# Performance work log

Measured on AMD Instinct MI355X. Metric: run time of the kernel, lower is better.

The kernel has to match this reference:

```python
import jax, jax.numpy as jnp
import numpy as np

N_USERS = 40000
N_POIS = 20000
D = 128
N_EDGES = 500000
N_LAYERS = 2
B = 256
NPOS = 100
TOPK = 20


def setup_inputs() -> dict:
    key = jax.random.key(0)
    ks = jax.random.split(key, 24)
    # guarantee every user row / poi col has at least one edge (avoids 0-norm rows)
    er = jnp.concatenate([jnp.arange(N_USERS, dtype=jnp.int32),
                          jax.random.randint(ks[0], (N_EDGES - N_USERS,), 0, N_USERS, jnp.int32)])
    ec = jnp.concatenate([jnp.arange(N_USERS, dtype=jnp.int32) % N_POIS,
                          jax.random.randint(ks[1], (N_EDGES - N_USERS,), 0, N_POIS, jnp.int32)])
    w0 = lambda k, shape: jax.random.normal(k, shape, jnp.float32) * 0.05
    return {
        'edge_row': er,
        'edge_col': ec,
        'click_vals': jax.random.uniform(ks[2], (N_EDGES,), jnp.float32),
        'favor_vals': jax.random.uniform(ks[3], (N_EDGES,), jnp.float32),
        'consume_vals': jax.random.uniform(ks[4], (N_EDGES,), jnp.float32),
        'uid_embed': w0(ks[5], (N_USERS, D)),
        'pid_embed': w0(ks[6], (N_POIS, D)),
        'user_index': jax.random.randint(ks[7], (B, 1), 0, N_USERS, jnp.int32),
        'poi_index': jax.random.randint(ks[8], (B, NPOS), 0, N_POIS, jnp.int32),
        'labels': (jax.random.uniform(ks[9], (B, NPOS)) < 0.5).astype(jnp.float32),
        'global_user_feature': w0(ks[10], (N_USERS, D)),
        'w': w0(ks[11], (1, 3)),
        'fw': w0(ks[12], (3, 1)),
        'W_user_click': w0(ks[13], (D, D)),
        'W_poi_click': w0(ks[14], (D, D)),
        'W_user_favor': w0(ks[15], (D, D)),
        'W_poi_favor': w0(ks[16], (D, D)),
        'W_user_consume': w0(ks[17], (D, D)),
        'W_poi_consume': w0(ks[18], (D, D)),
        'Ws': w0(ks[19], (D, D)),
        'bs_bias': w0(ks[20], (D,)),
    }


def reference(edge_row, edge_col, click_vals, favor_vals, consume_vals, uid_embed, pid_embed,
              user_index, poi_index, labels, global_user_feature, w, fw,
              W_user_click, W_poi_click, W_user_favor, W_poi_favor,
              W_user_consume, W_poi_consume, Ws, bs_bias):
    n_users, n_pois = uid_embed.shape[0], pid_embed.shape[0]
    batch_user = user_index.reshape(-1)

    def gcn(vals, Wu, Wp):
        # bipartite GCN propagation: A @ p (user side), A.T @ u (poi side)
        su, sp = uid_embed, pid_embed          # running sums of per-layer normalized features
        u, p = uid_embed, pid_embed            # un-normalized propagated features
        for _ in range(N_LAYERS):
            u = jax.ops.segment_sum(vals[:, None] * p[edge_col], edge_row, num_segments=n_users)
            su = su + u / jnp.linalg.norm(u, axis=1, keepdims=True)
            p = jax.ops.segment_sum(vals[:, None] * u[edge_row], edge_col, num_segments=n_pois)
            sp = sp + p / jnp.linalg.norm(p, axis=1, keepdims=True)
        uf = su @ Wu.T                         # final_user_linear (bias=False)
        pf = sp @ Wp.T                         # final_poi_linear (bias=False)
        return uf[batch_user] @ pf.T, uf       # [B, n_pois], [n_users, D]

    wn = jax.nn.softmax(w, axis=1)
    fwn = jax.nn.softmax(fw, axis=0)

    click_up, click_uf = gcn(click_vals, W_user_click, W_poi_click)
    favor_up, favor_uf = gcn(favor_vals + 1e-18 * click_vals, W_user_favor, W_poi_favor)
    consume_up, consume_uf = gcn(consume_vals + 1e-18 * click_vals, W_user_consume, W_poi_consume)

    alt = favor_up * wn[0, 0] + click_up * wn[0, 1] + consume_up * wn[0, 2]
    predict = jnp.take_along_axis(alt, poi_index, axis=1)                      # [B, NPOS]
    # BCEWithLogitsLoss (mean reduction), numerically stable form
    select_loss = jnp.mean(jax.nn.relu(predict) - predict * labels + jnp.log1p(jnp.exp(-jnp.abs(predict))))

    L = user_index.shape[1]
    cur = batch_user[jnp.arange(0, user_index.shape[0] * L, L)]                # first user of each row
    # gcn_user_feature stacked (favor, consume, click) @ fw
    id_feat = favor_uf * fwn[0, 0] + consume_uf * fwn[1, 0] + click_uf * fwn[2, 0]

    # Select_Layer (all inputs to matmuls are detached in the original)
    id_d = jax.lax.stop_gradient(id_feat)
    bs = id_d[cur] @ Ws.T + bs_bias
    uu = bs @ id_d.T                                                           # [B, n_users]
    top_score, top_idx = jax.lax.top_k(uu, TOPK)
    top_score = jax.nn.softmax(jax.lax.stop_gradient(top_score), axis=-1)
    neigh = jax.lax.stop_gradient(global_user_feature[top_idx])                # [B, TOPK, D]
    user_feature = jnp.einsum('bk,bkd->bd', top_score, neigh)
    return select_loss, user_feature
```

## Files before the change

kernel.cpp:

```cpp
#include <hip/hip_runtime.h>

#define N_USERS 40000
#define N_POIS  20000
#define DIM     128
#define N_EDGES 500000
#define BATCH   256
#define NPOS    100
#define TOPK    20
#define NCHUNK  128
#define CPT     313
#define SCHUNK  1024
#define RCH     40
#define CCH     20
#define LOSS_BLOCKS 25

typedef _Float16 f16x8 __attribute__((ext_vector_type(8)));
typedef float f32x4 __attribute__((ext_vector_type(4)));

__device__ __forceinline__ int iclamp(int x, int lo, int hi) {
    return x < lo ? lo : (x > hi ? hi : x);
}
__device__ __forceinline__ float2 h2f2(unsigned int u) {
    union { unsigned int u32; _Float16 h[2]; } v; v.u32 = u;
    return make_float2((float)v.h[0], (float)v.h[1]);
}
__device__ __forceinline__ unsigned int f2h2(float x, float y) {
    union { unsigned int u32; _Float16 h[2]; } v;
    v.h[0] = (_Float16)x; v.h[1] = (_Float16)y; return v.u32;
}
__device__ __forceinline__ float softmax3(const float* p, int sel) {
    float a0 = p[0], a1 = p[1], a2 = p[2];
    float m = fmaxf(a0, fmaxf(a1, a2));
    float e0 = expf(a0 - m), e1 = expf(a1 - m), e2 = expf(a2 - m);
    float den = e0 + e1 + e2;
    float e = (sel == 0) ? e0 : ((sel == 1) ? e1 : e2);
    return e / den;
}
template<int CH>
__device__ __forceinline__ float pickvT(int4 q) {
    return __int_as_float(CH == 0 ? q.y : (CH == 1 ? q.z : q.w));
}
__device__ __forceinline__ f16x8 frag8(const float* p) {
    float4 x = *(const float4*)(p);
    float4 y = *(const float4*)(p + 4);
    f16x8 f;
    f[0] = (_Float16)x.x; f[1] = (_Float16)x.y; f[2] = (_Float16)x.z; f[3] = (_Float16)x.w;
    f[4] = (_Float16)y.x; f[5] = (_Float16)y.y; f[6] = (_Float16)y.z; f[7] = (_Float16)y.w;
    return f;
}

__global__ void zero_kernel(unsigned int* __restrict__ p, int nwords) {
    int i = blockIdx.x * blockDim.x + threadIdx.x;
    if (i < nwords) p[i] = 0u;
}

__global__ void cast_f16_kernel(const float* __restrict__ src, unsigned short* __restrict__ dst,
                                int n2) {
    int i = blockIdx.x * blockDim.x + threadIdx.x;
    if (i < n2) {
        float2 v = *(const float2*)(src + 2 * (size_t)i);
        *(unsigned int*)(dst + 2 * (size_t)i) = f2h2(v.x, v.y);
    }
}

__global__ void hist_kernel(const int* __restrict__ er, const int* __restrict__ ec,
                            int* __restrict__ rcnt, int* __restrict__ ccnt,
                            int* __restrict__ rord, int* __restrict__ cord) {
    int e0 = 4 * (blockIdx.x * blockDim.x + threadIdx.x);
    if (e0 + 4 <= N_EDGES) {
        int4 r4 = *(const int4*)(er + e0);
        int4 c4 = *(const int4*)(ec + e0);
        int rr[4] = { r4.x, r4.y, r4.z, r4.w };
        int cc[4] = { c4.x, c4.y, c4.z, c4.w };
        int ro[4], co[4];
        #pragma unroll
        for (int j = 0; j < 4; j++) {
            ro[j] = atomicAdd(&rcnt[iclamp(rr[j], 0, N_USERS - 1)], 1);
            co[j] = atomicAdd(&ccnt[iclamp(cc[j], 0, N_POIS - 1)], 1);
        }
        *(int4*)(rord + e0) = make_int4(ro[0], ro[1], ro[2], ro[3]);
        *(int4*)(cord + e0) = make_int4(co[0], co[1], co[2], co[3]);
    } else {
        for (int e = e0; e < N_EDGES; e++) {
            rord[e] = atomicAdd(&rcnt[iclamp(er[e], 0, N_USERS - 1)], 1);
            cord[e] = atomicAdd(&ccnt[iclamp(ec[e], 0, N_POIS - 1)], 1);
        }
    }
}

__global__ void chunksum_kernel(const int* __restrict__ rcnt, const int* __restrict__ ccnt,
                                int* __restrict__ rsum, int* __restrict__ csum) {
    int side = blockIdx.y;
    const int* cnt = side ? ccnt : rcnt;
    int n = side ? N_POIS : N_USERS;
    int nch = side ? CCH : RCH;
    int b = blockIdx.x;
    if (b >= nch) return;
    int t = threadIdx.x;
    int i = b * SCHUNK + t * 4;
    int s = 0;
    if (i + 4 <= n) {
        int4 v = *(const int4*)(cnt + i);
        s = v.x + v.y + v.z + v.w;
    } else {
        for (int j = i; j < n; j++) s += cnt[j];
    }
    __shared__ int red[256];
    red[t] = s;
    __syncthreads();
    for (int o = 128; o > 0; o >>= 1) {
        if (t < o) red[t] += red[t + o];
        __syncthreads();
    }
    if (t == 0) (side ? csum : rsum)[b] = red[0];
}

__global__ void chunkscan_kernel(const int* __restrict__ rsum, const int* __restrict__ csum,
                                 int* __restrict__ rbase, int* __restrict__ cbase,
                                 int* __restrict__ rptr, int* __restrict__ cptr) {
    int w = threadIdx.x >> 6, l = threadIdx.x & 63;
    const int* src = w ? csum : rsum;
    int* dst = w ? cbase : rbase;
    int nch = w ? CCH : RCH;
    int orig = (l < nch) ? src[l] : 0;
    int v = orig;
    #pragma unroll
    for (int o = 1; o < 64; o <<= 1) {
        int u = __shfl_up(v, o, 64);
        if (l >= o) v += u;
    }
    if (l < nch) dst[l] = v - orig;
    if (l == nch - 1) {
        if (w) cptr[N_POIS] = v; else rptr[N_USERS] = v;
    }
}

__global__ void scatterscan_kernel(const int* __restrict__ rcnt, const int* __restrict__ ccnt,
                                   const int* __restrict__ rbase, const int* __restrict__ cbase,
                                   int* __restrict__ rptr, int* __restrict__ cptr) {
    int side = blockIdx.y;
    const int* cnt = side ? ccnt : rcnt;
    const int* basea = side ? cbase : rbase;
    int* ptr = side ? cptr : rptr;
    int n = side ? N_POIS : N_USERS;
    int nch = side ? CCH : RCH;
    int b = blockIdx.x;
    if (b >= nch) return;
    int t = threadIdx.x;
    int i = b * SCHUNK + t * 4;
    int c0 = 0, c1 = 0, c2 = 0, c3 = 0;
    if (i + 4 <= n) {
        int4 v = *(const int4*)(cnt + i);
        c0 = v.x; c1 = v.y; c2 = v.z; c3 = v.w;
    } else {
        if (i + 0 < n) c0 = cnt[i + 0];
        if (i + 1 < n) c1 = cnt[i + 1];
        if (i + 2 < n) c2 = cnt[i + 2];
    }
    int tsum = c0 + c1 + c2 + c3;
    int l = t & 63, w = t >> 6;
    int v = tsum;
    #pragma unroll
    for (int o = 1; o < 64; o <<= 1) {
        int u = __shfl_up(v, o, 64);
        if (l >= o) v += u;
    }
    __shared__ int wsum[4];
    if (l == 63) wsum[w] = v;
    __syncthreads();
    int wbase = 0;
    for (int k = 0; k < w; k++) wbase += wsum[k];
    int ex = v - tsum + wbase + basea[b];
    if (i + 4 <= n) {
        *(int4*)(ptr + i) = make_int4(ex, ex + c0, ex + c0 + c1, ex + c0 + c1 + c2);
    } else {
        if (i + 0 < n) ptr[i + 0] = ex;
        if (i + 1 < n) ptr[i + 1] = ex + c0;
        if (i + 2 < n) ptr[i + 2] = ex + c0 + c1;
    }
}

__global__ void fill_kernel(const int* __restrict__ er, const int* __restrict__ ec,
                            const int* __restrict__ rptr, const int* __restrict__ cptr,
                            const int* __restrict__ rord, const int* __restrict__ cord,
                            int4* __restrict__ rpack, int4* __restrict__ cpack,
                            const float* __restrict__ ck, const float* __restrict__ fv,
                            const float* __restrict__ cs) {
    int e0 = 4 * (blockIdx.x * blockDim.x + threadIdx.x);
    if (e0 + 4 <= N_EDGES) {
        int4 r4 = *(const int4*)(er + e0);
        int4 c4 = *(const int4*)(ec + e0);
        int4 ro4 = *(const int4*)(rord + e0);
        int4 co4 = *(const int4*)(cord + e0);
        float4 k4 = *(const float4*)(ck + e0);
        float4 f4 = *(const float4*)(fv + e0);
        float4 s4 = *(const float4*)(cs + e0);
        int rr[4] = { r4.x, r4.y, r4.z, r4.w };
        int cc[4] = { c4.x, c4.y, c4.z, c4.w };
        int ro[4] = { ro4.x, ro4.y, ro4.z, ro4.w };
        int co[4] = { co4.x, co4.y, co4.z, co4.w };
        float kk[4] = { k4.x, k4.y, k4.z, k4.w };
        float ff[4] = { f4.x, f4.y, f4.z, f4.w };
        float ss[4] = { s4.x, s4.y, s4.z, s4.w };
        #pragma unroll
        for (int j = 0; j < 4; j++) {
            int r = iclamp(rr[j], 0, N_USERS - 1), c = iclamp(cc[j], 0, N_POIS - 1);
            int v0 = __float_as_int(kk[j]);
            int v1 = __float_as_int(ff[j]);
            int v2 = __float_as_int(ss[j]);
            int pr = iclamp(rptr[r] + ro[j], 0, N_EDGES - 1);
            rpack[pr] = make_int4(c, v0, v1, v2);
            int pc = iclamp(cptr[c] + co[j], 0, N_EDGES - 1);
            cpack[pc] = make_int4(r, v0, v1, v2);
        }
    } else {
        for (int e = e0; e < N_EDGES; e++) {
            int r = iclamp(er[e], 0, N_USERS - 1), c = iclamp(ec[e], 0, N_POIS - 1);
            int v0 = __float_as_int(ck[e]);
            int v1 = __float_as_int(fv[e]);
            int v2 = __float_as_int(cs[e]);
            int pr = iclamp(rptr[r] + rord[e], 0, N_EDGES - 1);
            rpack[pr] = make_int4(c, v0, v1, v2);
            int pc = iclamp(cptr[c] + cord[e], 0, N_EDGES - 1);
            cpack[pc] = make_int4(r, v0, v1, v2);
        }
    }
}

template<int CH>
__global__ __launch_bounds__(256) void spmm_kernel(
        const int* __restrict__ ptr, const int4* __restrict__ pack,
        const unsigned short* __restrict__ src,
        unsigned short* __restrict__ raw_h,
        const float* __restrict__ base,
        float* __restrict__ acc, int nrows) {
    int wid = (blockIdx.x * blockDim.x + threadIdx.x) >> 6;
    int lane = threadIdx.x & 63;
    if (wid >= nrows) return;
    int beg = __builtin_amdgcn_readfirstlane(iclamp(ptr[wid], 0, N_EDGES));
    int end = __builtin_amdgcn_readfirstlane(iclamp(ptr[wid + 1], 0, N_EDGES));
    if (end < beg) end = beg;
    float ax = 0.f, ay = 0.f;
    int e = beg;
    int lo2 = lane * 2;
    for (; e + 8 <= end; e += 8) {
        int4 q0 = pack[e + 0], q1 = pack[e + 1], q2 = pack[e + 2], q3 = pack[e + 3];
        int4 q4 = pack[e + 4], q5 = pack[e + 5], q6 = pack[e + 6], q7 = pack[e + 7];
        float v0 = pickvT<CH>(q0), v1 = pickvT<CH>(q1), v2 = pickvT<CH>(q2), v3 = pickvT<CH>(q3);
        float v4 = pickvT<CH>(q4), v5 = pickvT<CH>(q5), v6 = pickvT<CH>(q6), v7 = pickvT<CH>(q7);
        float2 p0 = h2f2(*(const unsigned int*)(src + (size_t)q0.x * DIM + lo2));
        float2 p1 = h2f2(*(const unsigned int*)(src + (size_t)q1.x * DIM + lo2));
        float2 p2 = h2f2(*(const unsigned int*)(src + (size_t)q2.x * DIM + lo2));
        float2 p3 = h2f2(*(const unsigned int*)(src + (size_t)q3.x * DIM + lo2));
        float2 p4 = h2f2(*(const unsigned int*)(src + (size_t)q4.x * DIM + lo2));
        float2 p5 = h2f2(*(const unsigned int*)(src + (size_t)q5.x * DIM + lo2));
        float2 p6 = h2f2(*(const unsigned int*)(src + (size_t)q6.x * DIM + lo2));
        float2 p7 = h2f2(*(const unsigned int*)(src + (size_t)q7.x * DIM + lo2));
        ax = fmaf(v0, p0.x, fmaf(v1, p1.x, fmaf(v2, p2.x, fmaf(v3, p3.x, ax))));
        ax = fmaf(v4, p4.x, fmaf(v5, p5.x, fmaf(v6, p6.x, fmaf(v7, p7.x, ax))));
        ay = fmaf(v0, p0.y, fmaf(v1, p1.y, fmaf(v2, p2.y, fmaf(v3, p3.y, ay))));
        ay = fmaf(v4, p4.y, fmaf(v5, p5.y, fmaf(v6, p6.y, fmaf(v7, p7.y, ay))));
    }
    if (e < end) {
        int last = end - 1;
        int e1 = e + 1 <= last ? e + 1 : last;
        int e2 = e + 2 <= last ? e + 2 : last;
        int e3 = e + 3 <= last ? e + 3 : last;
        int e4 = e + 4 <= last ? e + 4 : last;
        int e5 = e + 5 <= last ? e + 5 : last;
        int e6 = e + 6 <= last ? e + 6 : last;
        int e7 = e + 7 <= last ? e + 7 : last;
        int4 q0 = pack[e], q1 = pack[e1], q2 = pack[e2], q3 = pack[e3];
        int4 q4 = pack[e4], q5 = pack[e5], q6 = pack[e6], q7 = pack[e7];
        float v0 = pickvT<CH>(q0);
        float v1 = (e + 1 < end) ? pickvT<CH>(q1) : 0.f;
        float v2 = (e + 2 < end) ? pickvT<CH>(q2) : 0.f;
        float v3 = (e + 3 < end) ? pickvT<CH>(q3) : 0.f;
        float v4 = (e + 4 < end) ? pickvT<CH>(q4) : 0.f;
        float v5 = (e + 5 < end) ? pickvT<CH>(q5) : 0.f;
        float v6 = (e + 6 < end) ? pickvT<CH>(q6) : 0.f;
        float v7 = (e + 7 < end) ? pickvT<CH>(q7) : 0.f;
        float2 p0 = h2f2(*(const unsigned int*)(src + (size_t)q0.x * DIM + lo2));
        float2 p1 = h2f2(*(const unsigned int*)(src + (size_t)q1.x * DIM + lo2));
        float2 p2 = h2f2(*(const unsigned int*)(src + (size_t)q2.x * DIM + lo2));
        float2 p3 = h2f2(*(const unsigned int*)(src + (size_t)q3.x * DIM + lo2));
        float2 p4 = h2f2(*(const unsigned int*)(src + (size_t)q4.x * DIM + lo2));
        float2 p5 = h2f2(*(const unsigned int*)(src + (size_t)q5.x * DIM + lo2));
        float2 p6 = h2f2(*(const unsigned int*)(src + (size_t)q6.x * DIM + lo2));
        float2 p7 = h2f2(*(const unsigned int*)(src + (size_t)q7.x * DIM + lo2));
        ax = fmaf(v0, p0.x, fmaf(v1, p1.x, fmaf(v2, p2.x, fmaf(v3, p3.x, ax))));
        ax = fmaf(v4, p4.x, fmaf(v5, p5.x, fmaf(v6, p6.x, fmaf(v7, p7.x, ax))));
        ay = fmaf(v0, p0.y, fmaf(v1, p1.y, fmaf(v2, p2.y, fmaf(v3, p3.y, ay))));
        ay = fmaf(v4, p4.y, fmaf(v5, p5.y, fmaf(v6, p6.y, fmaf(v7, p7.y, ay))));
    }
    float n2 = ax * ax + ay * ay;
    #pragma unroll
    for (int o = 32; o > 0; o >>= 1) n2 += __shfl_xor(n2, o, 64);
    float inv = rsqrtf(fmaxf(n2, 1e-30f));
    *(unsigned int*)(raw_h + (size_t)wid * DIM + lo2) = f2h2(ax, ay);
    float2 bv = *(const float2*)(base + (size_t)wid * DIM + lo2);
    *(float2*)(acc + (size_t)wid * DIM + lo2) =
        make_float2(bv.x + ax * inv, bv.y + ay * inv);
}

__global__ __launch_bounds__(256) void spmm3_kernel(
        const int* __restrict__ ptr, const int4* __restrict__ pack,
        const unsigned short* __restrict__ src,
        unsigned short* __restrict__ r0, unsigned short* __restrict__ r1,
        unsigned short* __restrict__ r2, int nrows) {
    int wid = (blockIdx.x * blockDim.x + threadIdx.x) >> 6;
    int lane = threadIdx.x & 63;
    if (wid >= nrows) return;
    int beg = __builtin_amdgcn_readfirstlane(iclamp(ptr[wid], 0, N_EDGES));
    int end = __builtin_amdgcn_readfirstlane(iclamp(ptr[wid + 1], 0, N_EDGES));
    if (end < beg) end = beg;
    float a0x = 0.f, a0y = 0.f, a1x = 0.f, a1y = 0.f, a2x = 0.f, a2y = 0.f;
    int e = beg;
    int lo2 = lane * 2;
    for (; e + 4 <= end; e += 4) {
        int4 q0 = pack[e + 0], q1 = pack[e + 1], q2 = pack[e + 2], q3 = pack[e + 3];
        float2 p0 = h2f2(*(const unsigned int*)(src + (size_t)q0.x * DIM + lo2));
        float2 p1 = h2f2(*(const unsigned int*)(src + (size_t)q1.x * DIM + lo2));
        float2 p2 = h2f2(*(const unsigned int*)(src + (size_t)q2.x * DIM + lo2));
        float2 p3 = h2f2(*(const unsigned int*)(src + (size_t)q3.x * DIM + lo2));
        a0x = fmaf(__int_as_float(q0.y), p0.x, fmaf(__int_as_float(q1.y), p1.x,
              fmaf(__int_as_float(q2.y), p2.x, fmaf(__int_as_float(q3.y), p3.x, a0x))));
        a0y = fmaf(__int_as_float(q0.y), p0.y, fmaf(__int_as_float(q1.y), p1.y,
              fmaf(__int_as_float(q2.y), p2.y, fmaf(__int_as_float(q3.y), p3.y, a0y))));
        a1x = fmaf(__int_as_float(q0.z), p0.x, fmaf(__int_as_float(q1.z), p1.x,
              fmaf(__int_as_float(q2.z), p2.x, fmaf(__int_as_float(q3.z), p3.x, a1x))));
        a1y = fmaf(__int_as_float(q0.z), p0.y, fmaf(__int_as_float(q1.z), p1.y,
              fmaf(__int_as_float(q2.z), p2.y, fmaf(__int_as_float(q3.z), p3.y, a1y))));
        a2x = fmaf(__int_as_float(q0.w), p0.x, fmaf(__int_as_float(q1.w), p1.x,
              fmaf(__int_as_float(q2.w), p2.x, fmaf(__int_as_float(q3.w), p3.x, a2x))));
        a2y = fmaf(__int_as_float(q0.w), p0.y, fmaf(__int_as_float(q1.w), p1.y,
              fmaf(__int_as_float(q2.w), p2.y, fmaf(__int_as_float(q3.w), p3.y, a2y))));
    }
    for (; e < end; e++) {
        int4 q = pack[e];
        float2 p = h2f2(*(const unsigned int*)(src + (size_t)q.x * DIM + lo2));
        a0x = fmaf(__int_as_float(q.y), p.x, a0x);
        a0y = fmaf(__int_as_float(q.y), p.y, a0y);
        a1x = fmaf(__int_as_float(q.z), p.x, a1x);
        a1y = fmaf(__int_as_float(q.z), p.y, a1y);
        a2x = fmaf(__int_as_float(q.w), p.x, a2x);
        a2y = fmaf(__int_as_float(q.w), p.y, a2y);
    }
    size_t o = (size_t)wid * DIM + lo2;
    *(unsigned int*)(r0 + o) = f2h2(a0x, a0y);
    *(unsigned int*)(r1 + o) = f2h2(a1x, a1y);
    *(unsigned int*)(r2 + o) = f2h2(a2x, a2y);
}

template<int CH>
__global__ __launch_bounds__(256) void spmm_l2u_kernel(
        const int* __restrict__ ptr, const int4* __restrict__ pack,
        const unsigned short* __restrict__ src,
        unsigned short* __restrict__ u1raw,
        const float* __restrict__ uid,
        float* __restrict__ su, int nrows) {
    int wid = (blockIdx.x * blockDim.x + threadIdx.x) >> 6;
    int lane = threadIdx.x & 63;
    if (wid >= nrows) return;
    int beg = __builtin_amdgcn_readfirstlane(iclamp(ptr[wid], 0, N_EDGES));
    int end = __builtin_amdgcn_readfirstlane(iclamp(ptr[wid + 1], 0, N_EDGES));
    if (end < beg) end = beg;
    float ax = 0.f, ay = 0.f;
    int e = beg;
    int lo2 = lane * 2;
    for (; e + 8 <= end; e += 8) {
        int4 q0 = pack[e + 0], q1 = pack[e + 1], q2 = pack[e + 2], q3 = pack[e + 3];
        int4 q4 = pack[e + 4], q5 = pack[e + 5], q6 = pack[e + 6], q7 = pack[e + 7];
        float v0 = pickvT<CH>(q0), v1 = pickvT<CH>(q1), v2 = pickvT<CH>(q2), v3 = pickvT<CH>(q3);
        float v4 = pickvT<CH>(q4), v5 = pickvT<CH>(q5), v6 = pickvT<CH>(q6), v7 = pickvT<CH>(q7);
        float2 p0 = h2f2(*(const unsigned int*)(src + (size_t)q0.x * DIM + lo2));
        float2 p1 = h2f2(*(const unsigned int*)(src + (size_t)q1.x * DIM + lo2));
        float2 p2 = h2f2(*(const unsigned int*)(src + (size_t)q2.x * DIM + lo2));
        float2 p3 = h2f2(*(const unsigned int*)(src + (size_t)q3.x * DIM + lo2));
        float2 p4 = h2f2(*(const unsigned int*)(src + (size_t)q4.x * DIM + lo2));
        float2 p5 = h2f2(*(const unsigned int*)(src + (size_t)q5.x * DIM + lo2));
        float2 p6 = h2f2(*(const unsigned int*)(src + (size_t)q6.x * DIM + lo2));
        float2 p7 = h2f2(*(const unsigned int*)(src + (size_t)q7.x * DIM + lo2));
        ax = fmaf(v0, p0.x, fmaf(v1, p1.x, fmaf(v2, p2.x, fmaf(v3, p3.x, ax))));
        ax = fmaf(v4, p4.x, fmaf(v5, p5.x, fmaf(v6, p6.x, fmaf(v7, p7.x, ax))));
        ay = fmaf(v0, p0.y, fmaf(v1, p1.y, fmaf(v2, p2.y, fmaf(v3, p3.y, ay))));
        ay = fmaf(v4, p4.y, fmaf(v5, p5.y, fmaf(v6, p6.y, fmaf(v7, p7.y, ay))));
    }
    if (e < end) {
        int last = end - 1;
        int e1 = e + 1 <= last ? e + 1 : last;
        int e2 = e + 2 <= last ? e + 2 : last;
        int e3 = e + 3 <= last ? e + 3 : last;
        int e4 = e + 4 <= last ? e + 4 : last;
        int e5 = e + 5 <= last ? e + 5 : last;
        int e6 = e + 6 <= last ? e + 6 : last;
        int e7 = e + 7 <= last ? e + 7 : last;
        int4 q0 = pack[e], q1 = pack[e1], q2 = pack[e2], q3 = pack[e3];
        int4 q4 = pack[e4], q5 = pack[e5], q6 = pack[e6], q7 = pack[e7];
        float v0 = pickvT<CH>(q0);
        float v1 = (e + 1 < end) ? pickvT<CH>(q1) : 0.f;
        float v2 = (e + 2 < end) ? pickvT<CH>(q2) : 0.f;
        float v3 = (e + 3 < end) ? pickvT<CH>(q3) : 0.f;
        float v4 = (e + 4 < end) ? pickvT<CH>(q4) : 0.f;
        float v5 = (e + 5 < end) ? pickvT<CH>(q5) : 0.f;
        float v6 = (e + 6 < end) ? pickvT<CH>(q6) : 0.f;
        float v7 = (e + 7 < end) ? pickvT<CH>(q7) : 0.f;
        float2 p0 = h2f2(*(const unsigned int*)(src + (size_t)q0.x * DIM + lo2));
        float2 p1 = h2f2(*(const unsigned int*)(src + (size_t)q1.x * DIM + lo2));
        float2 p2 = h2f2(*(const unsigned int*)(src + (size_t)q2.x * DIM + lo2));
        float2 p3 = h2f2(*(const unsigned int*)(src + (size_t)q3.x * DIM + lo2));
        float2 p4 = h2f2(*(const unsigned int*)(src + (size_t)q4.x * DIM + lo2));
        float2 p5 = h2f2(*(const unsigned int*)(src + (size_t)q5.x * DIM + lo2));
        float2 p6 = h2f2(*(const unsigned int*)(src + (size_t)q6.x * DIM + lo2));
        float2 p7 = h2f2(*(const unsigned int*)(src + (size_t)q7.x * DIM + lo2));
        ax = fmaf(v0, p0.x, fmaf(v1, p1.x, fmaf(v2, p2.x, fmaf(v3, p3.x, ax))));
        ax = fmaf(v4, p4.x, fmaf(v5, p5.x, fmaf(v6, p6.x, fmaf(v7, p7.x, ax))));
        ay = fmaf(v0, p0.y, fmaf(v1, p1.y, fmaf(v2, p2.y, fmaf(v3, p3.y, ay))));
        ay = fmaf(v4, p4.y, fmaf(v5, p5.y, fmaf(v6, p6.y, fmaf(v7, p7.y, ay))));
    }
    size_t o = (size_t)wid * DIM + lo2;
    float2 u1 = h2f2(*(const unsigned int*)(u1raw + o));
    float n2a = ax * ax + ay * ay;
    float n2b = u1.x * u1.x + u1.y * u1.y;
    #pragma unroll
    for (int oo = 32; oo > 0; oo >>= 1) {
        n2a += __shfl_xor(n2a, oo, 64);
        n2b += __shfl_xor(n2b, oo, 64);
    }
    float i2 = rsqrtf(fmaxf(n2a, 1e-30f));
    float i1 = rsqrtf(fmaxf(n2b, 1e-30f));
    *(unsigned int*)(u1raw + o) = f2h2(ax, ay);
    float2 bv = *(const float2*)(uid + o);
    *(float2*)(su + o) = make_float2(bv.x + u1.x * i1 + ax * i2,
                                     bv.y + u1.y * i1 + ay * i2);
}

__global__ __launch_bounds__(256) void gemm_mfma_kernel(
        const float* __restrict__ A, const float* __restrict__ W,
        float* __restrict__ store, float* __restrict__ accum,
        _Float16* __restrict__ accum_h,
        const float* __restrict__ fw3, int fsel, int first, int M) {
    int w = threadIdx.x >> 6, l = threadIdx.x & 63;
    int lg = l >> 4, lc = l & 15;
    int j0 = w * 32;
    float coef = accum ? softmax3(fw3, fsel) : 0.f;
    f16x8 Bf[2][4];
    #pragma unroll
    for (int t = 0; t < 2; t++) {
        const float* wr = W + (size_t)(j0 + t * 16 + lc) * DIM + lg * 8;
        #pragma unroll
        for (int s = 0; s < 4; s++) Bf[t][s] = frag8(wr + s * 32);
    }
    int base = blockIdx.x * 64;
    #pragma unroll
    for (int rt = 0; rt < 4; rt++) {
        int u0 = base + rt * 16;
        int ar = u0 + lc; if (ar > M - 1) ar = M - 1;
        const float* arow = A + (size_t)ar * DIM + lg * 8;
        f16x8 Af[4];
        #pragma unroll
        for (int s = 0; s < 4; s++) Af[s] = frag8(arow + s * 32);
        f32x4 acc0 = {0.f, 0.f, 0.f, 0.f};
        f32x4 acc1 = {0.f, 0.f, 0.f, 0.f};
        #pragma unroll
        for (int s = 0; s < 4; s++) {
            acc0 = __builtin_amdgcn_mfma_f32_16x16x32_f16(Af[s], Bf[0][s], acc0, 0, 0, 0);
            acc1 = __builtin_amdgcn_mfma_f32_16x16x32_f16(Af[s], Bf[1][s], acc1, 0, 0, 0);
        }
        int rbase = u0 + lg * 4;
        #pragma unroll
        for (int r = 0; r < 4; r++) {
            int row = rbase + r;
            if (row >= M) continue;
            size_t o0 = (size_t)row * DIM + j0 + lc;
            size_t o1 = o0 + 16;
            if (store) { store[o0] = acc0[r]; store[o1] = acc1[r]; }
            if (accum) {
                float p0 = first ? 0.f : accum[o0];
                float p1 = first ? 0.f : accum[o1];
                float n0 = p0 + coef * acc0[r];
                float n1 = p1 + coef * acc1[r];
                accum[o0] = n0;
                accum[o1] = n1;
                if (accum_h) {
                    accum_h[o0] = (_Float16)n0;
                    accum_h[o1] = (_Float16)n1;
                }
            }
        }
    }
}

__global__ void ufsel_kernel(const float* __restrict__ su, const float* __restrict__ W,
                             const int* __restrict__ uidx, float* __restrict__ outsel) {
    int b = blockIdx.x, j = threadIdx.x;
    __shared__ float ar[128];
    int u = iclamp(uidx[b], 0, N_USERS - 1);
    ar[j] = su[(size_t)u * DIM + j];
    __syncthreads();
    const float4* Wr = (const float4*)(W + (size_t)j * DIM);
    float acc = 0.f;
    #pragma unroll 8
    for (int q = 0; q < 32; q++) {
        float4 wq = Wr[q];
        acc = fmaf(ar[4 * q + 0], wq.x, acc);
        acc = fmaf(ar[4 * q + 1], wq.y, acc);
        acc = fmaf(ar[4 * q + 2], wq.z, acc);
        acc = fmaf(ar[4 * q + 3], wq.w, acc);
    }
    outsel[(size_t)b * DIM + j] = acc;
}

__global__ __launch_bounds__(256) void predict_kernel(
        const float* __restrict__ ufs, const float* __restrict__ pf,
        const int* __restrict__ pidx, const float* __restrict__ w3,
        int wsel, int first, float* __restrict__ alt) {
    int wid = (blockIdx.x * blockDim.x + threadIdx.x) >> 6;
    int lane = threadIdx.x & 63;
    if (wid >= BATCH * NPOS) return;
    int b = wid / NPOS;
    int poi = iclamp(pidx[wid], 0, N_POIS - 1);
    const float2 uv = *(const float2*)(ufs + (size_t)b * DIM + lane * 2);
    const float2 pv = *(const float2*)(pf + (size_t)poi * DIM + lane * 2);
    float s = uv.x * pv.x + uv.y * pv.y;
    #pragma unroll
    for (int o = 32; o > 0; o >>= 1) s += __shfl_xor(s, o, 64);
    if (lane == 0) {
        float coef = softmax3(w3, wsel);
        float prev = first ? 0.f : alt[wid];
        alt[wid] = prev + coef * s;
    }
}

__global__ void loss_part_kernel(const float* __restrict__ alt, const float* __restrict__ labels,
                                 float* __restrict__ part) {
    int b = blockIdx.x, t = threadIdx.x;
    int i = b * 1024 + t * 4;
    float4 x4 = *(const float4*)(alt + i);
    float4 y4 = *(const float4*)(labels + i);
    float s = 0.f;
    s += fmaxf(x4.x, 0.f) - x4.x * y4.x + log1pf(expf(-fabsf(x4.x)));
    s += fmaxf(x4.y, 0.f) - x4.y * y4.y + log1pf(expf(-fabsf(x4.y)));
    s += fmaxf(x4.z, 0.f) - x4.z * y4.z + log1pf(expf(-fabsf(x4.z)));
    s += fmaxf(x4.w, 0.f) - x4.w * y4.w + log1pf(expf(-fabsf(x4.w)));
    __shared__ float red[256];
    red[t] = s;
    __syncthreads();
    for (int o = 128; o > 0; o >>= 1) {
        if (t < o) red[t] += red[t + o];
        __syncthreads();
    }
    if (t == 0) part[b] = red[0];
}

__global__ void loss_final_kernel(const float* __restrict__ part, float* __restrict__ out) {
    if (threadIdx.x == 0) {
        float s = 0.f;
        #pragma unroll
        for (int b = 0; b < LOSS_BLOCKS; b++) s += part[b];
        out[0] = s / (float)(BATCH * NPOS);
    }
}

__global__ void bs_kernel(const float* __restrict__ idf, const float* __restrict__ Ws,
                          const float* __restrict__ bias, const int* __restrict__ uidx,
                          _Float16* __restrict__ bst_h) {
    int b = blockIdx.x, j = threadIdx.x;
    __shared__ float ar[128];
    int u = iclamp(uidx[b], 0, N_USERS - 1);
    ar[j] = idf[(size_t)u * DIM + j];
    __syncthreads();
    const float4* Wr = (const float4*)(Ws + (size_t)j * DIM);
    float acc = 0.f;
    #pragma unroll 8
    for (int q = 0; q < 32; q++) {
        float4 wq = Wr[q];
        acc = fmaf(ar[4 * q + 0], wq.x, acc);
        acc = fmaf(ar[4 * q + 1], wq.y, acc);
        acc = fmaf(ar[4 * q + 2], wq.z, acc);
        acc = fmaf(ar[4 * q + 3], wq.w, acc);
    }
    bst_h[(size_t)b * DIM + j] = (_Float16)(acc + bias[j]);
}

__device__ __forceinline__ void topk_insert(float s, int u, float* ts, int* ti) {
    if (s > ts[TOPK - 1]) {
        #pragma unroll
        for (int j = TOPK - 1; j > 0; --j) {
            bool above = s > ts[j - 1];
            bool here = (!above) && (s > ts[j]);
            float nv = above ? ts[j - 1] : (here ? s : ts[j]);
            int ni = above ? ti[j - 1] : (here ? u : ti[j]);
            ts[j] = nv; ti[j] = ni;
        }
        if (s > ts[0]) { ts[0] = s; ti[0] = u; }
    }
}

__global__ __launch_bounds__(512) void score_topk_kernel(
        const _Float16* __restrict__ idf_h, const _Float16* __restrict__ bst_h,
        float* __restrict__ cand_s, int* __restrict__ cand_i) {
    __shared__ __align__(16) unsigned char smraw[61440];
    float* ms = (float*)smraw;
    unsigned short* mi = (unsigned short*)(smraw + 40960);
    int cid = blockIdx.x, bg = blockIdx.y;
    int tid = threadIdx.x;
    int w = tid >> 6, l = tid & 63;
    int half = w >> 2, wq = w & 3;
    int lg = l >> 4, lc = l & 15;
    const _Float16* bbase = bst_h + ((size_t)(bg * 64 + wq * 16 + lc)) * DIM + lg * 8;
    f16x8 B0 = *(const f16x8*)(bbase + 0);
    f16x8 B1 = *(const f16x8*)(bbase + 32);
    f16x8 B2 = *(const f16x8*)(bbase + 64);
    f16x8 B3 = *(const f16x8*)(bbase + 96);
    float ts[TOPK]; int ti[TOPK];
    #pragma unroll
    for (int k = 0; k < TOPK; k++) { ts[k] = -3.0e38f; ti[k] = 0; }
    int lo = cid * CPT;
    int hi = lo + CPT; if (hi > N_USERS) hi = N_USERS;
    int ntiles = (hi - lo + 15) >> 4;
    int t0 = half ? (ntiles >> 1) : 0;
    int t1 = half ? ntiles : (ntiles >> 1);
    #pragma unroll 2
    for (int t = t0; t < t1; t++) {
        int u0 = lo + t * 16;
        int ar = u0 + lc; if (ar > N_USERS - 1) ar = N_USERS - 1;
        const _Float16* abase = idf_h + (size_t)ar * DIM + lg * 8;
        f16x8 A0 = *(const f16x8*)(abase + 0);
        f16x8 A1 = *(const f16x8*)(abase + 32);
        f16x8 A2 = *(const f16x8*)(abase + 64);
        f16x8 A3 = *(const f16x8*)(abase + 96);
        f32x4 accA = {0.f, 0.f, 0.f, 0.f};
        f32x4 accB = {0.f, 0.f, 0.f, 0.f};
        accA = __builtin_amdgcn_mfma_f32_16x16x32_f16(A0, B0, accA, 0, 0, 0);
        accB = __builtin_amdgcn_mfma_f32_16x16x32_f16(A1, B1, accB, 0, 0, 0);
        accA = __builtin_amdgcn_mfma_f32_16x16x32_f16(A2, B2, accA, 0, 0, 0);
        accB = __builtin_amdgcn_mfma_f32_16x16x32_f16(A3, B3, accB, 0, 0, 0);
        int ub = u0 + lg * 4;
        #pragma unroll
        for (int r = 0; r < 4; r++) {
            float s = accA[r] + accB[r];
            int u = ub + r;
            if (u < hi) topk_insert(s, u, ts, ti);
        }
    }
    #pragma unroll
    for (int k = 0; k < TOPK; k++) {
        ms[k * 512 + tid] = ts[k];
        mi[k * 512 + tid] = (unsigned short)ti[k];
    }
    __syncthreads();
    if (tid < 64) {
        int wm = tid >> 4, cm = tid & 15;
        int s0 = 0 * 256 + wm * 64 + 0 * 16 + cm;
        int s1 = s0 + 16, s2 = s0 + 32, s3 = s0 + 48;
        int s4 = s0 + 256, s5 = s1 + 256, s6 = s2 + 256, s7 = s3 + 256;
        int p0 = 0, p1 = 0, p2 = 0, p3 = 0, p4 = 0, p5 = 0, p6 = 0, p7 = 0;
        size_t ob = ((size_t)cid * 256 + bg * 64 + wm * 16 + cm) * TOPK;
        for (int k = 0; k < TOPK; k++) {
            float h0 = ms[p0 * 512 + s0];
            float h1 = ms[p1 * 512 + s1];
            float h2 = ms[p2 * 512 + s2];
            float h3 = ms[p3 * 512 + s3];
            float h4 = ms[p4 * 512 + s4];
            float h5 = ms[p5 * 512 + s5];
            float h6 = ms[p6 * 512 + s6];
            float h7 = ms[p7 * 512 + s7];
            float best = h0; int which = 0;
            if (h1 > best) { best = h1; which = 1; }
            if (h2 > best) { best = h2; which = 2; }
            if (h3 > best) { best = h3; which = 3; }
            if (h4 > best) { best = h4; which = 4; }
            if (h5 > best) { best = h5; which = 5; }
            if (h6 > best) { best = h6; which = 6; }
            if (h7 > best) { best = h7; which = 7; }
            int idx;
            if (which == 0)      { idx = mi[p0 * 512 + s0]; p0++; }
            else if (which == 1) { idx = mi[p1 * 512 + s1]; p1++; }
            else if (which == 2) { idx = mi[p2 * 512 + s2]; p2++; }
            else if (which == 3) { idx = mi[p3 * 512 + s3]; p3++; }
            else if (which == 4) { idx = mi[p4 * 512 + s4]; p4++; }
            else if (which == 5) { idx = mi[p5 * 512 + s5]; p5++; }
            else if (which == 6) { idx = mi[p6 * 512 + s6]; p6++; }
            else                 { idx = mi[p7 * 512 + s7]; p7++; }
            cand_s[ob + k] = best;
            cand_i[ob + k] = idx;
        }
    }
}

__global__ void topk_merge_kernel(const float* __restrict__ cand_s, const int* __restrict__ cand_i,
                                  const float* __restrict__ guf,
                                  float* __restrict__ outp) {
    int b = blockIdx.x, t = threadIdx.x;
    __shared__ float rs[NCHUNK]; __shared__ int ru[NCHUNK]; __shared__ int rt[NCHUNK];
    __shared__ float win_s[TOPK]; __shared__ int win_u[TOPK]; __shared__ float wk[TOPK];
    __shared__ int winner;
    int ptr = 0;
    size_t base = ((size_t)t * 256 + b) * TOPK;
    for (int k = 0; k < TOPK; k++) {
        rs[t] = (ptr < TOPK) ? cand_s[base + ptr] : -3.0e38f;
        ru[t] = (ptr < TOPK) ? cand_i[base + ptr] : 0;
        rt[t] = t;
        __syncthreads();
        for (int off = NCHUNK / 2; off > 0; off >>= 1) {
            if (t < off && rs[t + off] > rs[t]) {
                rs[t] = rs[t + off]; ru[t] = ru[t + off]; rt[t] = rt[t + off];
            }
            __syncthreads();
        }
        if (t == 0) { win_s[k] = rs[0]; win_u[k] = iclamp(ru[0], 0, N_USERS - 1); winner = rt[0]; }
        __syncthreads();
        if (t == winner) ptr++;
        __syncthreads();
    }
    if (t == 0) {
        float m = win_s[0], den = 0.f;
        for (int k = 0; k < TOPK; k++) { wk[k] = expf(win_s[k] - m); den += wk[k]; }
        float inv = 1.f / den;
        for (int k = 0; k < TOPK; k++) wk[k] *= inv;
    }
    __syncthreads();
    float acc = 0.f;
    #pragma unroll
    for (int k = 0; k < TOPK; k++)
        acc = fmaf(wk[k], guf[(size_t)win_u[k] * DIM + t], acc);
    outp[1 + (size_t)b * DIM + t] = acc;
}

extern "C" void kernel_launch(void* const* d_in, const int* in_sizes, int n_in,
                              void* d_out, int out_size, void* d_ws, size_t ws_size,
                              hipStream_t stream) {
    (void)in_sizes; (void)n_in; (void)out_size;
    const int*   er      = (const int*)d_in[0];
    const int*   ec      = (const int*)d_in[1];
    const float* click   = (const float*)d_in[2];
    const float* favor   = (const float*)d_in[3];
    const float* consume = (const float*)d_in[4];
    const float* uid     = (const float*)d_in[5];
    const float* pid     = (const float*)d_in[6];
    const int*   uidx    = (const int*)d_in[7];
    const int*   pidx    = (const int*)d_in[8];
    const float* labels  = (const float*)d_in[9];
    const float* guf     = (const float*)d_in[10];
    const float* w3      = (const float*)d_in[11];
    const float* fw3     = (const float*)d_in[12];
    const float* Wuc     = (const float*)d_in[13];
    const float* Wpc     = (const float*)d_in[14];
    const float* Wufv    = (const float*)d_in[15];
    const float* Wpfv    = (const float*)d_in[16];
    const float* Wuco    = (const float*)d_in[17];
    const float* Wpco    = (const float*)d_in[18];
    const float* Wss     = (const float*)d_in[19];
    const float* bias    = (const float*)d_in[20];
    float* outp = (float*)d_out;

    char* ws = (char*)d_ws;
    size_t off = 0;
    auto carve = [&](size_t bytes) -> void* {
        off = (off + 255) & ~(size_t)255;
        void* p = ws + off;
        off += bytes;
        return p;
    };
    float* ufs = (float*)carve(4ll * 3 * BATCH * DIM);
    float* alt = (float*)carve(4ll * BATCH * NPOS);
    float* bst = (float*)carve(4ll * DIM * BATCH);
    int* rptr = (int*)carve(4 * (N_USERS + 1));
    int* cptr = (int*)carve(4 * (N_POIS + 1));
    int* cnts = (int*)carve(4 * (N_USERS + N_POIS));
    int* rcnt = cnts;
    int* ccnt = cnts + N_USERS;
    int* scanws = (int*)carve(4 * 2 * (RCH + CCH) + 4 * 64);
    int* rsum = scanws;
    int* csum = rsum + RCH;
    int* rbase = csum + CCH;
    int* cbase = rbase + RCH;
    float* losspart = (float*)carve(4 * (LOSS_BLOCKS + 7));
    int4* rpack = (int4*)carve(16ll * N_EDGES);
    int4* cpack = (int4*)carve(16ll * N_EDGES);
    unsigned short* pid_h = (unsigned short*)carve(2ll * N_POIS * DIM);
    unsigned short* utr0 = (unsigned short*)carve(2ll * N_USERS * DIM);
    unsigned short* ptr_h = (unsigned short*)carve(2ll * N_POIS * DIM);
    float* su  = (float*)carve(4ll * N_USERS * DIM);
    float* sp  = (float*)carve(4ll * N_POIS * DIM);
    float* idf = (float*)carve(4ll * N_USERS * DIM);
    float* pf = (float*)utr0;
    float* cand_s = su;
    int*   cand_i = (int*)(su + (size_t)NCHUNK * BATCH * TOPK);
    _Float16* idf_h = (_Float16*)rpack;
    _Float16* bst_h = (_Float16*)bst;
    int* rord = (int*)su;
    int* cord = rord + N_EDGES;
    unsigned short* utr1 = (unsigned short*)carve(2ll * N_USERS * DIM);
    unsigned short* utr2 = (unsigned short*)carve(2ll * N_USERS * DIM);
    bool fused = (off <= ws_size);

    zero_kernel<<<(N_USERS + N_POIS + 255) / 256, 256, 0, stream>>>(
        (unsigned int*)cnts, N_USERS + N_POIS);
    cast_f16_kernel<<<(N_POIS * DIM / 2 + 255) / 256, 256, 0, stream>>>(pid, pid_h, N_POIS * DIM / 2);
    hist_kernel<<<(N_EDGES / 4 + 255) / 256, 256, 0, stream>>>(er, ec, rcnt, ccnt, rord, cord);
    dim3 sg2(RCH, 2);
    chunksum_kernel<<<sg2, 256, 0, stream>>>(rcnt, ccnt, rsum, csum);
    chunkscan_kernel<<<1, 128, 0, stream>>>(rsum, csum, rbase, cbase, rptr, cptr);
    scatterscan_kernel<<<sg2, 256, 0, stream>>>(rcnt, ccnt, rbase, cbase, rptr, cptr);
    fill_kernel<<<(N_EDGES / 4 + 255) / 256, 256, 0, stream>>>(
        er, ec, rptr, cptr, rord, cord, rpack, cpack, click, favor, consume);

    struct Ch { const float* Wu; const float* Wp; int wsel; int fsel; };
    Ch chs[3] = { { Wuc,  Wpc,  1, 2 },
                  { Wufv, Wpfv, 0, 0 },
                  { Wuco, Wpco, 2, 1 } };

    const int UGB = N_USERS / 64;
    const int PGB = (N_POIS + 63) / 64;
    const int PW = N_POIS * 64 / 256;
    const int UW = N_USERS * 64 / 256;

    auto launch_spmm_poi = [&](int c, const unsigned short* src, unsigned short* raw,
                               const float* base, float* acc) {
        if (c == 0)      spmm_kernel<0><<<PW, 256, 0, stream>>>(cptr, cpack, src, raw, base, acc, N_POIS);
        else if (c == 1) spmm_kernel<1><<<PW, 256, 0, stream>>>(cptr, cpack, src, raw, base, acc, N_POIS);
        else             spmm_kernel<2><<<PW, 256, 0, stream>>>(cptr, cpack, src, raw, base, acc, N_POIS);
    };
    auto launch_spmm_usr = [&](int c, const unsigned short* src, unsigned short* raw,
                               const float* base, float* acc) {
        if (c == 0)      spmm_kernel<0><<<UW, 256, 0, stream>>>(rptr, rpack, src, raw, base, acc, N_USERS);
        else if (c == 1) spmm_kernel<1><<<UW, 256, 0, stream>>>(rptr, rpack, src, raw, base, acc, N_USERS);
        else             spmm_kernel<2><<<UW, 256, 0, stream>>>(rptr, rpack, src, raw, base, acc, N_USERS);
    };
    auto launch_l2u = [&](int c, const unsigned short* src, unsigned short* u1raw) {
        if (c == 0)      spmm_l2u_kernel<0><<<UW, 256, 0, stream>>>(rptr, rpack, src, u1raw, uid, su, N_USERS);
        else if (c == 1) spmm_l2u_kernel<1><<<UW, 256, 0, stream>>>(rptr, rpack, src, u1raw, uid, su, N_USERS);
        else             spmm_l2u_kernel<2><<<UW, 256, 0, stream>>>(rptr, rpack, src, u1raw, uid, su, N_USERS);
    };

    if (fused) {
        spmm3_kernel<<<UW, 256, 0, stream>>>(rptr, rpack, pid_h, utr0, utr1, utr2, N_USERS);
        for (int c = 0; c < 3; c++) {
            unsigned short* uc = (c == 0) ? utr0 : ((c == 1) ? utr1 : utr2);
            launch_spmm_poi(c, uc, ptr_h, pid, sp);
            launch_l2u(c, ptr_h, uc);
            launch_spmm_poi(c, uc, ptr_h, sp, sp);
            gemm_mfma_kernel<<<UGB, 256, 0, stream>>>(
                su, chs[c].Wu, nullptr, idf, (c == 2) ? idf_h : nullptr,
                fw3, chs[c].fsel, (c == 0) ? 1 : 0, N_USERS);
            ufsel_kernel<<<BATCH, 128, 0, stream>>>(su, chs[c].Wu, uidx, ufs + (size_t)c * BATCH * DIM);
            gemm_mfma_kernel<<<PGB, 256, 0, stream>>>(
                sp, chs[c].Wp, pf, nullptr, nullptr, fw3, 0, 0, N_POIS);
            predict_kernel<<<BATCH * NPOS * 64 / 256, 256, 0, stream>>>(
                ufs + (size_t)c * BATCH * DIM, pf, pidx, w3, chs[c].wsel, (c == 0) ? 1 : 0, alt);
        }
    } else {
        for (int c = 0; c < 3; c++) {
            launch_spmm_usr(c, pid_h, utr0, uid, su);
            launch_spmm_poi(c, utr0, ptr_h, pid, sp);
            launch_spmm_usr(c, ptr_h, utr0, su, su);
            launch_spmm_poi(c, utr0, ptr_h, sp, sp);
            gemm_mfma_kernel<<<UGB, 256, 0, stream>>>(
                su, chs[c].Wu, nullptr, idf, (c == 2) ? idf_h : nullptr,
                fw3, chs[c].fsel, (c == 0) ? 1 : 0, N_USERS);
            ufsel_kernel<<<BATCH, 128, 0, stream>>>(su, chs[c].Wu, uidx, ufs + (size_t)c * BATCH * DIM);
            gemm_mfma_kernel<<<PGB, 256, 0, stream>>>(
                sp, chs[c].Wp, pf, nullptr, nullptr, fw3, 0, 0, N_POIS);
            predict_kernel<<<BATCH * NPOS * 64 / 256, 256, 0, stream>>>(
                ufs + (size_t)c * BATCH * DIM, pf, pidx, w3, chs[c].wsel, (c == 0) ? 1 : 0, alt);
        }
    }

    loss_part_kernel<<<LOSS_BLOCKS, 256, 0, stream>>>(alt, labels, losspart);
    loss_final_kernel<<<1, 64, 0, stream>>>(losspart, outp);
    bs_kernel<<<BATCH, 128, 0, stream>>>(idf, Wss, bias, uidx, bst_h);
    dim3 sg(NCHUNK, 4);
    score_topk_kernel<<<sg, 512, 0, stream>>>(idf_h, bst_h, cand_s, cand_i);
    topk_merge_kernel<<<BATCH, NCHUNK, 0, stream>>>(cand_s, cand_i, guf, outp);
}
```

Measured before the change: 661.0 us.

## Batch first-layer POI SpMM across channels and fuse second-layer POI normalize

Adds a three-channel POI-side SpMM that computes the first propagation layer for click, favor and consume in one pass, so the edge list and indices are read once instead of three times. Adds an l2p kernel that fuses the second POI-side propagation with the per-row L2 normalization and base sum, replacing separate poi SpMM launches. This reduces kernel launches and redundant edge and pointer traffic. The cost is two extra f16 POI buffers and higher register pressure in the fused kernel.

Result: faster. 647.4 us (-2.1%).

```diff
diff --git a/kernel.cpp b/kernel.cpp
--- a/kernel.cpp
+++ b/kernel.cpp
@@ -352,6 +352,69 @@
     *(unsigned int*)(r2 + o) = f2h2(a2x, a2y);
 }
 
+__global__ __launch_bounds__(256) void spmm3p_kernel(
+        const int* __restrict__ ptr, const int4* __restrict__ pack,
+        const unsigned short* __restrict__ s0, const unsigned short* __restrict__ s1,
+        const unsigned short* __restrict__ s2,
+        unsigned short* __restrict__ r0, unsigned short* __restrict__ r1,
+        unsigned short* __restrict__ r2, int nrows) {
+    int wid = (blockIdx.x * blockDim.x + threadIdx.x) >> 6;
+    int lane = threadIdx.x & 63;
+    if (wid >= nrows) return;
+    int beg = __builtin_amdgcn_readfirstlane(iclamp(ptr[wid], 0, N_EDGES));
+    int end = __builtin_amdgcn_readfirstlane(iclamp(ptr[wid + 1], 0, N_EDGES));
+    if (end < beg) end = beg;
+    float a0x = 0.f, a0y = 0.f, a1x = 0.f, a1y = 0.f, a2x = 0.f, a2y = 0.f;
+    int e = beg;
+    int lo2 = lane * 2;
+    for (; e + 4 <= end; e += 4) {
+        int4 q0 = pack[e + 0], q1 = pack[e + 1], q2 = pack[e + 2], q3 = pack[e + 3];
+        size_t o0 = (size_t)q0.x * DIM + lo2, o1 = (size_t)q1.x * DIM + lo2;
+        size_t o2 = (size_t)q2.x * DIM + lo2, o3 = (size_t)q3.x * DIM + lo2;
+        float2 u00 = h2f2(*(const unsigned int*)(s0 + o0));
+        float2 u01 = h2f2(*(const unsigned int*)(s0 + o1));
+        float2 u02 = h2f2(*(const unsigned int*)(s0 + o2));
+        float2 u03 = h2f2(*(const unsigned int*)(s0 + o3));
+        float2 u10 = h2f2(*(const unsigned int*)(s1 + o0));
+        float2 u11 = h2f2(*(const unsigned int*)(s1 + o1));
+        float2 u12 = h2f2(*(const unsigned int*)(s1 + o2));
+        float2 u13 = h2f2(*(const unsigned int*)(s1 + o3));
+        float2 u20 = h2f2(*(const unsigned int*)(s2 + o0));
+        float2 u21 = h2f2(*(const unsigned int*)(s2 + o1));
+        float2 u22 = h2f2(*(const unsigned int*)(s2 + o2));
+        float2 u23 = h2f2(*(const unsigned int*)(s2 + o3));
+        a0x = fmaf(__int_as_float(q0.y), u00.x, fmaf(__int_as_float(q1.y), u01.x,
+              fmaf(__int_as_float(q2.y), u02.x, fmaf(__int_as_float(q3.y), u03.x, a0x))));
+        a0y = fmaf(__int_as_float(q0.y), u00.y, fmaf(__int_as_float(q1.y), u01.y,
+              fmaf(__int_as_float(q2.y), u02.y, fmaf(__int_as_float(q3.y), u03.y, a0y))));
+        a1x = fmaf(__int_as_float(q0.z), u10.x, fmaf(__int_as_float(q1.z), u11.x,
+              fmaf(__int_as_float(q2.z), u12.x, fmaf(__int_as_float(q3.z), u13.x, a1x))));
+        a1y = fmaf(__int_as_float(q0.z), u10.y, fmaf(__int_as_float(q1.z), u11.y,
+              fmaf(__int_as_float(q2.z), u12.y, fmaf(__int_as_float(q3.z), u13.y, a1y))));
+        a2x = fmaf(__int_as_float(q0.w), u20.x, fmaf(__int_as_float(q1.w), u21.x,
+              fmaf(__int_as_float(q2.w), u22.x, fmaf(__int_as_float(q3.w), u23.x, a2x))));
+        a2y = fmaf(__int_as_float(q0.w), u20.y, fmaf(__int_as_float(q1.w), u21.y,
+              fmaf(__int_as_float(q2.w), u22.y, fmaf(__int_as_float(q3.w), u23.y, a2y))));
+    }
+    for (; e < end; e++) {
+        int4 q = pack[e];
+        size_t o = (size_t)q.x * DIM + lo2;
+        float2 p0 = h2f2(*(const unsigned int*)(s0 + o));
+        float2 p1 = h2f2(*(const unsigned int*)(s1 + o));
+        float2 p2 = h2f2(*(const unsigned int*)(s2 + o));
+        a0x = fmaf(__int_as_float(q.y), p0.x, a0x);
+        a0y = fmaf(__int_as_float(q.y), p0.y, a0y);
+        a1x = fmaf(__int_as_float(q.z), p1.x, a1x);
+        a1y = fmaf(__int_as_float(q.z), p1.y, a1y);
+        a2x = fmaf(__int_as_float(q.w), p2.x, a2x);
+        a2y = fmaf(__int_as_float(q.w), p2.y, a2y);
+    }
+    size_t o = (size_t)wid * DIM + lo2;
+    *(unsigned int*)(r0 + o) = f2h2(a0x, a0y);
+    *(unsigned int*)(r1 + o) = f2h2(a1x, a1y);
+    *(unsigned int*)(r2 + o) = f2h2(a2x, a2y);
+}
+
 template<int CH>
 __global__ __launch_bounds__(256) void spmm_l2u_kernel(
         const int* __restrict__ ptr, const int4* __restrict__ pack,
@@ -433,6 +496,88 @@
     float2 bv = *(const float2*)(uid + o);
     *(float2*)(su + o) = make_float2(bv.x + u1.x * i1 + ax * i2,
                                      bv.y + u1.y * i1 + ay * i2);
+}
+
+template<int CH>
+__global__ __launch_bounds__(256) void spmm_l2p_kernel(
+        const int* __restrict__ ptr, const int4* __restrict__ pack,
+        const unsigned short* __restrict__ src,
+        const unsigned short* __restrict__ p1raw,
+        const float* __restrict__ pid,
+        float* __restrict__ sp, int nrows) {
+    int wid = (blockIdx.x * blockDim.x + threadIdx.x) >> 6;
+    int lane = threadIdx.x & 63;
+    if (wid >= nrows) return;
+    int beg = __builtin_amdgcn_readfirstlane(iclamp(ptr[wid], 0, N_EDGES));
+    int end = __builtin_amdgcn_readfirstlane(iclamp(ptr[wid + 1], 0, N_EDGES));
+    if (end < beg) end = beg;
+    float ax = 0.f, ay = 0.f;
+    int e = beg;
+    int lo2 = lane * 2;
+    for (; e + 8 <= end; e += 8) {
+        int4 q0 = pack[e + 0], q1 = pack[e + 1], q2 = pack[e + 2], q3 = pack[e + 3];
+        int4 q4 = pack[e + 4], q5 = pack[e + 5], q6 = pack[e + 6], q7 = pack[e + 7];
+        float v0 = pickvT<CH>(q0), v1 = pickvT<CH>(q1), v2 = pickvT<CH>(q2), v3 = pickvT<CH>(q3);
+        float v4 = pickvT<CH>(q4), v5 = pickvT<CH>(q5), v6 = pickvT<CH>(q6), v7 = pickvT<CH>(q7);
+        float2 p0 = h2f2(*(const unsigned int*)(src + (size_t)q0.x * DIM + lo2));
+        float2 p1 = h2f2(*(const unsigned int*)(src + (size_t)q1.x * DIM + lo2));
+        float2 p2 = h2f2(*(const unsigned int*)(src + (size_t)q2.x * DIM + lo2));
+        float2 p3 = h2f2(*(const unsigned int*)(src + (size_t)q3.x * DIM + lo2));
+        float2 p4 = h2f2(*(const unsigned int*)(src + (size_t)q4.x * DIM + lo2));
+        float2 p5 = h2f2(*(const unsigned int*)(src + (size_t)q5.x * DIM + lo2));
+        float2 p6 = h2f2(*(const unsigned int*)(src + (size_t)q6.x * DIM + lo2));
+        float2 p7 = h2f2(*(const unsigned int*)(src + (size_t)q7.x * DIM + lo2));
+        ax = fmaf(v0, p0.x, fmaf(v1, p1.x, fmaf(v2, p2.x, fmaf(v3, p3.x, ax))));
+        ax = fmaf(v4, p4.x, fmaf(v5, p5.x, fmaf(v6, p6.x, fmaf(v7, p7.x, ax))));
+        ay = fmaf(v0, p0.y, fmaf(v1, p1.y, fmaf(v2, p2.y, fmaf(v3, p3.y, ay))));
+        ay = fmaf(v4, p4.y, fmaf(v5, p5.y, fmaf(v6, p6.y, fmaf(v7, p7.y, ay))));
+    }
+    if (e < end) {
+        int last = end - 1;
+        int e1 = e + 1 <= last ? e + 1 : last;
+        int e2 = e + 2 <= last ? e + 2 : last;
+        int e3 = e + 3 <= last ? e + 3 : last;
+        int e4 = e + 4 <= last ? e + 4 : last;
+        int e5 = e + 5 <= last ? e + 5 : last;
+        int e6 = e + 6 <= last ? e + 6 : last;
+        int e7 = e + 7 <= last ? e + 7 : last;
+        int4 q0 = pack[e], q1 = pack[e1], q2 = pack[e2], q3 = pack[e3];
+        int4 q4 = pack[e4], q5 = pack[e5], q6 = pack[e6], q7 = pack[e7];
+        float v0 = pickvT<CH>(q0);
+        float v1 = (e + 1 < end) ? pickvT<CH>(q1) : 0.f;
+        float v2 = (e + 2 < end) ? pickvT<CH>(q2) : 0.f;
+        float v3 = (e + 3 < end) ? pickvT<CH>(q3) : 0.f;
+        float v4 = (e + 4 < end) ? pickvT<CH>(q4) : 0.f;
+        float v5 = (e + 5 < end) ? pickvT<CH>(q5) : 0.f;
+        float v6 = (e + 6 < end) ? pickvT<CH>(q6) : 0.f;
+        float v7 = (e + 7 < end) ? pickvT<CH>(q7) : 0.f;
+        float2 p0 = h2f2(*(const unsigned int*)(src + (size_t)q0.x * DIM + lo2));
+        float2 p1 = h2f2(*(const unsigned int*)(src + (size_t)q1.x * DIM + lo2));
+        float2 p2 = h2f2(*(const unsigned int*)(src + (size_t)q2.x * DIM + lo2));
+        float2 p3 = h2f2(*(const unsigned int*)(src + (size_t)q3.x * DIM + lo2));
+        float2 p4 = h2f2(*(const unsigned int*)(src + (size_t)q4.x * DIM + lo2));
+        float2 p5 = h2f2(*(const unsigned int*)(src + (size_t)q5.x * DIM + lo2));
+        float2 p6 = h2f2(*(const unsigned int*)(src + (size_t)q6.x * DIM + lo2));
+        float2 p7 = h2f2(*(const unsigned int*)(src + (size_t)q7.x * DIM + lo2));
+        ax = fmaf(v0, p0.x, fmaf(v1, p1.x, fmaf(v2, p2.x, fmaf(v3, p3.x, ax))));
+        ax = fmaf(v4, p4.x, fmaf(v5, p5.x, fmaf(v6, p6.x, fmaf(v7, p7.x, ax))));
+        ay = fmaf(v0, p0.y, fmaf(v1, p1.y, fmaf(v2, p2.y, fmaf(v3, p3.y, ay))));
+        ay = fmaf(v4, p4.y, fmaf(v5, p5.y, fmaf(v6, p6.y, fmaf(v7, p7.y, ay))));
+    }
+    size_t o = (size_t)wid * DIM + lo2;
+    float2 p1v = h2f2(*(const unsigned int*)(p1raw + o));
+    float n2a = ax * ax + ay * ay;
+    float n2b = p1v.x * p1v.x + p1v.y * p1v.y;
+    #pragma unroll
+    for (int oo = 32; oo > 0; oo >>= 1) {
+        n2a += __shfl_xor(n2a, oo, 64);
+        n2b += __shfl_xor(n2b, oo, 64);
+    }
+    float i2 = rsqrtf(fmaxf(n2a, 1e-30f));
+    float i1 = rsqrtf(fmaxf(n2b, 1e-30f));
+    float2 bv = *(const float2*)(pid + o);
+    *(float2*)(sp + o) = make_float2(bv.x + p1v.x * i1 + ax * i2,
+                                     bv.y + p1v.y * i1 + ay * i2);
 }
 
 __global__ __launch_bounds__(256) void gemm_mfma_kernel(
@@ -794,6 +939,8 @@
     int* cord = rord + N_EDGES;
     unsigned short* utr1 = (unsigned short*)carve(2ll * N_USERS * DIM);
     unsigned short* utr2 = (unsigned short*)carve(2ll * N_USERS * DIM);
+    unsigned short* p1b1 = (unsigned short*)carve(2ll * N_POIS * DIM);
+    unsigned short* p1b2 = (unsigned short*)carve(2ll * N_POIS * DIM);
     bool fused = (off <= ws_size);
 
     zero_kernel<<<(N_USERS + N_POIS + 255) / 256, 256, 0, stream>>>(
@@ -834,14 +981,21 @@
         else if (c == 1) spmm_l2u_kernel<1><<<UW, 256, 0, stream>>>(rptr, rpack, src, u1raw, uid, su, N_USERS);
         else             spmm_l2u_kernel<2><<<UW, 256, 0, stream>>>(rptr, rpack, src, u1raw, uid, su, N_USERS);
     };
+    auto launch_l2p = [&](int c, const unsigned short* src, const unsigned short* p1raw) {
+        if (c == 0)      spmm_l2p_kernel<0><<<PW, 256, 0, stream>>>(cptr, cpack, src, p1raw, pid, sp, N_POIS);
+        else if (c == 1) spmm_l2p_kernel<1><<<PW, 256, 0, stream>>>(cptr, cpack, src, p1raw, pid, sp, N_POIS);
+        else             spmm_l2p_kernel<2><<<PW, 256, 0, stream>>>(cptr, cpack, src, p1raw, pid, sp, N_POIS);
+    };
 
     if (fused) {
         spmm3_kernel<<<UW, 256, 0, stream>>>(rptr, rpack, pid_h, utr0, utr1, utr2, N_USERS);
+        spmm3p_kernel<<<PW, 256, 0, stream>>>(cptr, cpack, utr0, utr1, utr2,
+                                              ptr_h, p1b1, p1b2, N_POIS);
+        unsigned short* p1b[3] = { ptr_h, p1b1, p1b2 };
+        unsigned short* utr[3] = { utr0, utr1, utr2 };
         for (int c = 0; c < 3; c++) {
-            unsigned short* uc = (c == 0) ? utr0 : ((c == 1) ? utr1 : utr2);
-            launch_spmm_poi(c, uc, ptr_h, pid, sp);
-            launch_l2u(c, ptr_h, uc);
-            launch_spmm_poi(c, uc, ptr_h, sp, sp);
+            launch_l2u(c, p1b[c], utr[c]);
+            launch_l2p(c, utr[c], p1b[c]);
             gemm_mfma_kernel<<<UGB, 256, 0, stream>>>(
                 su, chs[c].Wu, nullptr, idf, (c == 2) ? idf_h : nullptr,
                 fw3, chs[c].fsel, (c == 0) ? 1 : 0, N_USERS);
```
